# Kernel optimization log

Hardware: AMD Instinct MI355X
Metric: run time of the kernel (lower is better)

The kernel has to match this reference:

```python
import jax, jax.numpy as jnp
import numpy as np

EPS = 1e-5


def setup_inputs() -> dict:
    key = jax.random.key(0)
    x = jax.random.normal(key, (16, 128, 513), dtype=jnp.float32)
    return {"x": x}


def reference(x):
    N, C, T = x.shape
    # split into even / odd time indices
    x1 = x[:, :, 0::2]                      # (N, C, t) with t = ceil(T/2)
    x2 = x[:, :, 1::2]                      # (N, C, p) with p = floor(T/2)
    # outer-product score: exp(x1)[...,t] * exp(-x2)[...,p]  -> (N, C, t, p)
    g = jnp.exp(x1)[:, :, :, None] * jnp.exp(-x2)[:, :, None, :]
    g = jnp.log(g + EPS) ** 2
    # mean over channels, then exp -> (N, t, p)
    RAM = jnp.exp(jnp.sum(g, axis=1) / C)
    # normalizeRAM: threshold + sum-based symmetric normalization
    RAM = jnp.where(RAM < 0.5, jnp.zeros_like(RAM), RAM)
    da = jnp.sum(RAM, axis=1)               # (N, p)  sum over t
    db = jnp.sum(RAM, axis=2)               # (N, t)  sum over p
    norm = (db[:, :, None] * da[:, None, :] + EPS) ** -0.5
    RAM = RAM * norm                         # (N, t, p)
    # upsample by 2 along both dims, drop last row -> (N, T, T-1)
    RAM = jnp.repeat(RAM, 2, axis=1)[:, :-1, :]
    RAM = jnp.repeat(RAM, 2, axis=2)
    # einsum 'nct,ntp->nct' == x * sum_p RAM
    return x * jnp.sum(RAM, axis=2)[:, None, :]
```

## Files before the change

### kernel.cpp

```cpp
#include <hip/hip_runtime.h>
#include <math.h>

#define N_B 16
#define C_CH 128
#define T_LEN 513
#define NI 257
#define NJ 256
#define NPD 9
#define SCALE (1.4426950408889634f/128.0f)

typedef unsigned u32;
typedef unsigned short u16;
typedef short bf16x8 __attribute__((ext_vector_type(8)));
typedef float f32x4 __attribute__((ext_vector_type(4)));

#define RAM_F 0
#define PDA_F (N_B*NI*NJ)

__device__ inline u32 cvtpk(float a, float b) {
    u32 r;
    asm("v_cvt_pk_bf16_f32 %0, %1, %2" : "=v"(r) : "v"(a), "v"(b));
    return r;
}

__device__ inline void cvt8(const float* fa, bf16x8& hv, bf16x8& lv) {
    union { u32 w[4]; bf16x8 v; } H, L;
    #pragma unroll
    for (int p = 0; p < 4; ++p) {
        const float a = fa[2*p], b = fa[2*p+1];
        const u32 h = cvtpk(a, b);
        const float la = a - __builtin_bit_cast(float, h << 16);
        const float lb = b - __builtin_bit_cast(float, h & 0xffff0000u);
        H.w[p] = h;
        L.w[p] = cvtpk(la, lb);
    }
    hv = H.v; lv = L.v;
}

__global__ __launch_bounds__(512, 2) void k1(const float* __restrict__ x,
                                             float* __restrict__ ram,
                                             float* __restrict__ pda) {
    __shared__ float As[64][132];
    __shared__ float Bs[64][132];
    const int jb = blockIdx.x, ib = blockIdx.y, n = blockIdx.z;
    const int i0 = ib * 64, j0 = jb * 64;
    const int tid = threadIdx.x;
    const int l = tid & 63, wv = tid >> 6;
    const float* xn = x + (size_t)n * (C_CH * T_LEN);
    float* rn = ram + (size_t)n * NI * NJ;

    {
        #pragma unroll
        for (int m = 0; m < 16; ++m) {
            const int c = wv * 16 + m;
            {
                const int idx = c * T_LEN + 2 * i0 + 2 * l;
                const float2 f2 = *(const float2*)(xn + (idx & ~1));
                As[l][c] = (idx & 1) ? f2.y : f2.x;
            }
            {
                const int idx = c * T_LEN + 2 * j0 + 2 * l + 1;
                const float2 f2 = *(const float2*)(xn + (idx & ~1));
                Bs[l][c] = (idx & 1) ? f2.y : f2.x;
            }
        }
    }
    __syncthreads();

    const int il = l & 15, g = l >> 4;
    const int ia = wv >> 2, jt = wv & 3;
    {
        bf16x8 ah[2][4], al[2][4], bh[4], bl[4];
        float psum[2] = {0.f, 0.f}, qsq = 0.f;
        #pragma unroll
        for (int kc = 0; kc < 4; ++kc) {
            float fb[8];
            const float* bp = &Bs[jt * 16 + il][kc * 32 + 8 * g];
            #pragma unroll
            for (int e = 0; e < 8; ++e) fb[e] = bp[e];
            #pragma unroll
            for (int e = 0; e < 8; ++e) qsq = fmaf(fb[e], fb[e], qsq);
            cvt8(fb, bh[kc], bl[kc]);
            #pragma unroll
            for (int s = 0; s < 2; ++s) {
                float fa[8];
                const float* ap = &As[ia * 32 + s * 16 + il][kc * 32 + 8 * g];
                #pragma unroll
                for (int e = 0; e < 8; ++e) fa[e] = ap[e];
                #pragma unroll
                for (int e = 0; e < 8; ++e) psum[s] = fmaf(fa[e], fa[e], psum[s]);
                cvt8(fa, ah[s][kc], al[s][kc]);
            }
        }
        #pragma unroll
        for (int s = 0; s < 2; ++s) {
            psum[s] += __shfl_xor(psum[s], 16, 64);
            psum[s] += __shfl_xor(psum[s], 32, 64);
        }
        qsq += __shfl_xor(qsq, 16, 64);
        qsq += __shfl_xor(qsq, 32, 64);
        float pv[2][4];
        #pragma unroll
        for (int s = 0; s < 2; ++s)
            #pragma unroll
            for (int r = 0; r < 4; ++r) pv[s][r] = __shfl(psum[s], 4 * g + r, 64);

        f32x4 acc[2];
        acc[0] = (f32x4){0.f, 0.f, 0.f, 0.f};
        acc[1] = (f32x4){0.f, 0.f, 0.f, 0.f};
        #pragma unroll
        for (int kc = 0; kc < 4; ++kc) {
            #pragma unroll
            for (int s = 0; s < 2; ++s) {
                acc[s] = __builtin_amdgcn_mfma_f32_16x16x32_bf16(ah[s][kc], bh[kc], acc[s], 0, 0, 0);
                acc[s] = __builtin_amdgcn_mfma_f32_16x16x32_bf16(ah[s][kc], bl[kc], acc[s], 0, 0, 0);
                acc[s] = __builtin_amdgcn_mfma_f32_16x16x32_bf16(al[s][kc], bh[kc], acc[s], 0, 0, 0);
            }
        }
        const int j = j0 + jt * 16 + il;
        float cs = 0.f;
        #pragma unroll
        for (int s = 0; s < 2; ++s) {
            #pragma unroll
            for (int r = 0; r < 4; ++r) {
                const int i = i0 + ia * 32 + s * 16 + 4 * g + r;
                const float rv = exp2f((pv[s][r] + qsq - 2.f * acc[s][r]) * SCALE);
                rn[(size_t)i * NJ + j] = rv;
                cs += rv;
            }
        }
        cs += __shfl_xor(cs, 16, 64);
        cs += __shfl_xor(cs, 32, 64);
        if (l < 16) pda[((size_t)n * NPD + ib * 2 + ia) * NJ + j0 + jt * 16 + l] = cs;
    }

    if (ib == 0) {
        const int jl = tid >> 3, sub = tid & 7;
        float sab = 0.f, saa = 0.f, sbb = 0.f;
        #pragma unroll
        for (int e = 0; e < 16; ++e) {
            const int c = sub * 16 + e;
            const float a = xn[c * T_LEN + 512];
            const float b = Bs[jl][c];
            sab = fmaf(a, b, sab);
            saa = fmaf(a, a, saa);
            sbb = fmaf(b, b, sbb);
        }
        #pragma unroll
        for (int o = 4; o; o >>= 1) {
            sab += __shfl_xor(sab, o, 64);
            saa += __shfl_xor(saa, o, 64);
            sbb += __shfl_xor(sbb, o, 64);
        }
        if (sub == 0) {
            const float rv = exp2f((saa + sbb - 2.f * sab) * SCALE);
            rn[(size_t)256 * NJ + j0 + jl] = rv;
            pda[((size_t)n * NPD + 8) * NJ + j0 + jl] = rv;
        }
    }
}

__global__ __launch_bounds__(256) void k2(const float* __restrict__ ram,
                                          const float* __restrict__ pda,
                                          const float* __restrict__ x,
                                          float* __restrict__ out) {
    const int ic = blockIdx.x, n = blockIdx.y;
    __shared__ float w_s[NJ];
    __shared__ float f_s[16];
    const int tid = threadIdx.x;
    {
        float da = 0.f;
        #pragma unroll
        for (int k = 0; k < NPD; ++k) da += pda[((size_t)n * NPD + k) * NJ + tid];
        w_s[tid] = rsqrtf(da);
    }
    __syncthreads();
    const int wv = tid >> 6, lane = tid & 63;
    #pragma unroll
    for (int rr = 0; rr < 4; ++rr) {
        const int lr = wv * 4 + rr;
        const int i = ic * 16 + lr;
        if (i < NI) {
            const float* rrow = ram + ((size_t)n * NI + i) * NJ;
            float db = 0.f, t0 = 0.f;
            #pragma unroll
            for (int k = 0; k < 4; ++k) {
                const float v = rrow[lane + 64 * k];
                db += v;
                t0 = fmaf(v, w_s[lane + 64 * k], t0);
            }
            #pragma unroll
            for (int off = 32; off; off >>= 1) {
                db += __shfl_xor(db, off, 64);
                t0 += __shfl_xor(t0, off, 64);
            }
            if (lane == 0) f_s[lr] = 2.f * t0 * rsqrtf(db);
        }
    }
    __syncthreads();
    const int tt = tid & 31, cgp = tid >> 5;
    const int t = ic * 32 + tt;
    if (t < T_LEN) {
        const float f = f_s[tt >> 1];
        const float* xn = x + (size_t)n * C_CH * T_LEN;
        float* on = out + (size_t)n * C_CH * T_LEN;
        #pragma unroll
        for (int p = 0; p < 16; ++p) {
            const int c = cgp * 16 + p;
            on[c * T_LEN + t] = xn[c * T_LEN + t] * f;
        }
    }
}

extern "C" void kernel_launch(void* const* d_in, const int* in_sizes, int n_in,
                              void* d_out, int out_size, void* d_ws, size_t ws_size,
                              hipStream_t stream) {
    const float* x = (const float*)d_in[0];
    float* out = (float*)d_out;
    float* ws = (float*)d_ws;
    float* ram = ws + RAM_F;
    float* pda = ws + PDA_F;

    k1<<<dim3(4, 4, N_B), 512, 0, stream>>>(x, ram, pda);
    k2<<<dim3(17, N_B), 256, 0, stream>>>(ram, pda, x, out);
}
```

Measured before the change: 19.35 us.

## Convert operands to split bf16 once at load and store bf16 tiles in LDS

Each element is now split into high and low bf16 parts once, while loading from global memory, and stored as bf16 tiles in shared memory. Previously each wave re-read fp32 tiles and converted them redundantly. Row squared norms are now reduced through shared memory instead of wave shuffles, and MFMA fragments are read with vector LDS loads. This cuts redundant conversion and halves LDS traffic. It adds an extra barrier and reconstructs the last-column B values from the hi+lo parts, which is slightly less precise than the original fp32.

```diff
diff --git a/kernel.cpp b/kernel.cpp
--- a/kernel.cpp
+++ b/kernel.cpp
@@ -13,6 +13,7 @@
 typedef unsigned short u16;
 typedef short bf16x8 __attribute__((ext_vector_type(8)));
 typedef float f32x4 __attribute__((ext_vector_type(4)));
+typedef u32 u32x4 __attribute__((ext_vector_type(4)));
 
 #define RAM_F 0
 #define PDA_F (N_B*NI*NJ)
@@ -23,25 +24,12 @@
     return r;
 }
 
-__device__ inline void cvt8(const float* fa, bf16x8& hv, bf16x8& lv) {
-    union { u32 w[4]; bf16x8 v; } H, L;
-    #pragma unroll
-    for (int p = 0; p < 4; ++p) {
-        const float a = fa[2*p], b = fa[2*p+1];
-        const u32 h = cvtpk(a, b);
-        const float la = a - __builtin_bit_cast(float, h << 16);
-        const float lb = b - __builtin_bit_cast(float, h & 0xffff0000u);
-        H.w[p] = h;
-        L.w[p] = cvtpk(la, lb);
-    }
-    hv = H.v; lv = L.v;
-}
-
 __global__ __launch_bounds__(512, 2) void k1(const float* __restrict__ x,
                                              float* __restrict__ ram,
                                              float* __restrict__ pda) {
-    __shared__ float As[64][132];
-    __shared__ float Bs[64][132];
+    __shared__ u16 Ah[64][136], Al[64][136], Bh[64][136], Bl[64][136];
+    __shared__ float PpT[8][64], QpT[8][64];
+    __shared__ float Ps[64], Qs[64];
     const int jb = blockIdx.x, ib = blockIdx.y, n = blockIdx.z;
     const int i0 = ib * 64, j0 = jb * 64;
     const int tid = threadIdx.x;
@@ -50,89 +38,102 @@
     float* rn = ram + (size_t)n * NI * NJ;
 
     {
+        float av[16], bv[16];
         #pragma unroll
         for (int m = 0; m < 16; ++m) {
             const int c = wv * 16 + m;
             {
                 const int idx = c * T_LEN + 2 * i0 + 2 * l;
                 const float2 f2 = *(const float2*)(xn + (idx & ~1));
-                As[l][c] = (idx & 1) ? f2.y : f2.x;
+                av[m] = (idx & 1) ? f2.y : f2.x;
             }
             {
                 const int idx = c * T_LEN + 2 * j0 + 2 * l + 1;
                 const float2 f2 = *(const float2*)(xn + (idx & ~1));
-                Bs[l][c] = (idx & 1) ? f2.y : f2.x;
-            }
-        }
-    }
-    __syncthreads();
+                bv[m] = (idx & 1) ? f2.y : f2.x;
+            }
+        }
+        float pp = 0.f, qq = 0.f;
+        u32 ahw[8], alw[8], bhw[8], blw[8];
+        #pragma unroll
+        for (int p = 0; p < 8; ++p) {
+            const float a0 = av[2*p], a1 = av[2*p+1];
+            const float b0 = bv[2*p], b1 = bv[2*p+1];
+            pp = fmaf(a0, a0, fmaf(a1, a1, pp));
+            qq = fmaf(b0, b0, fmaf(b1, b1, qq));
+            const u32 ha = cvtpk(a0, a1);
+            ahw[p] = ha;
+            alw[p] = cvtpk(a0 - __builtin_bit_cast(float, ha << 16),
+                           a1 - __builtin_bit_cast(float, ha & 0xffff0000u));
+            const u32 hb = cvtpk(b0, b1);
+            bhw[p] = hb;
+            blw[p] = cvtpk(b0 - __builtin_bit_cast(float, hb << 16),
+                           b1 - __builtin_bit_cast(float, hb & 0xffff0000u));
+        }
+        u32* d;
+        d = (u32*)&Ah[l][16 * wv]; *(u32x4*)d = *(u32x4*)&ahw[0]; *(u32x4*)(d + 4) = *(u32x4*)&ahw[4];
+        d = (u32*)&Al[l][16 * wv]; *(u32x4*)d = *(u32x4*)&alw[0]; *(u32x4*)(d + 4) = *(u32x4*)&alw[4];
+        d = (u32*)&Bh[l][16 * wv]; *(u32x4*)d = *(u32x4*)&bhw[0]; *(u32x4*)(d + 4) = *(u32x4*)&bhw[4];
+        d = (u32*)&Bl[l][16 * wv]; *(u32x4*)d = *(u32x4*)&blw[0]; *(u32x4*)(d + 4) = *(u32x4*)&blw[4];
+        PpT[wv][l] = pp;
+        QpT[wv][l] = qq;
+    }
+    __syncthreads();
+
+    if (tid < 64) {
+        float s = 0.f;
+        #pragma unroll
+        for (int w = 0; w < 8; ++w) s += PpT[w][tid];
+        Ps[tid] = s;
+    } else if (tid < 128) {
+        float s = 0.f;
+        #pragma unroll
+        for (int w = 0; w < 8; ++w) s += QpT[w][tid - 64];
+        Qs[tid - 64] = s;
+    }
 
     const int il = l & 15, g = l >> 4;
     const int ia = wv >> 2, jt = wv & 3;
-    {
-        bf16x8 ah[2][4], al[2][4], bh[4], bl[4];
-        float psum[2] = {0.f, 0.f}, qsq = 0.f;
-        #pragma unroll
-        for (int kc = 0; kc < 4; ++kc) {
-            float fb[8];
-            const float* bp = &Bs[jt * 16 + il][kc * 32 + 8 * g];
-            #pragma unroll
-            for (int e = 0; e < 8; ++e) fb[e] = bp[e];
-            #pragma unroll
-            for (int e = 0; e < 8; ++e) qsq = fmaf(fb[e], fb[e], qsq);
-            cvt8(fb, bh[kc], bl[kc]);
-            #pragma unroll
-            for (int s = 0; s < 2; ++s) {
-                float fa[8];
-                const float* ap = &As[ia * 32 + s * 16 + il][kc * 32 + 8 * g];
-                #pragma unroll
-                for (int e = 0; e < 8; ++e) fa[e] = ap[e];
-                #pragma unroll
-                for (int e = 0; e < 8; ++e) psum[s] = fmaf(fa[e], fa[e], psum[s]);
-                cvt8(fa, ah[s][kc], al[s][kc]);
-            }
-        }
+    bf16x8 fah[2][4], fal[2][4], fbh[4], fbl[4];
+    #pragma unroll
+    for (int kc = 0; kc < 4; ++kc) {
+        fbh[kc]    = *(const bf16x8*)&Bh[jt * 16 + il][kc * 32 + 8 * g];
+        fbl[kc]    = *(const bf16x8*)&Bl[jt * 16 + il][kc * 32 + 8 * g];
+        fah[0][kc] = *(const bf16x8*)&Ah[ia * 32 + il][kc * 32 + 8 * g];
+        fah[1][kc] = *(const bf16x8*)&Ah[ia * 32 + 16 + il][kc * 32 + 8 * g];
+        fal[0][kc] = *(const bf16x8*)&Al[ia * 32 + il][kc * 32 + 8 * g];
+        fal[1][kc] = *(const bf16x8*)&Al[ia * 32 + 16 + il][kc * 32 + 8 * g];
+    }
+    f32x4 acc[2];
+    acc[0] = (f32x4){0.f, 0.f, 0.f, 0.f};
+    acc[1] = (f32x4){0.f, 0.f, 0.f, 0.f};
+    #pragma unroll
+    for (int kc = 0; kc < 4; ++kc) {
         #pragma unroll
         for (int s = 0; s < 2; ++s) {
-            psum[s] += __shfl_xor(psum[s], 16, 64);
-            psum[s] += __shfl_xor(psum[s], 32, 64);
-        }
-        qsq += __shfl_xor(qsq, 16, 64);
-        qsq += __shfl_xor(qsq, 32, 64);
-        float pv[2][4];
-        #pragma unroll
-        for (int s = 0; s < 2; ++s)
-            #pragma unroll
-            for (int r = 0; r < 4; ++r) pv[s][r] = __shfl(psum[s], 4 * g + r, 64);
-
-        f32x4 acc[2];
-        acc[0] = (f32x4){0.f, 0.f, 0.f, 0.f};
-        acc[1] = (f32x4){0.f, 0.f, 0.f, 0.f};
-        #pragma unroll
-        for (int kc = 0; kc < 4; ++kc) {
-            #pragma unroll
-            for (int s = 0; s < 2; ++s) {
-                acc[s] = __builtin_amdgcn_mfma_f32_16x16x32_bf16(ah[s][kc], bh[kc], acc[s], 0, 0, 0);
-                acc[s] = __builtin_amdgcn_mfma_f32_16x16x32_bf16(ah[s][kc], bl[kc], acc[s], 0, 0, 0);
-                acc[s] = __builtin_amdgcn_mfma_f32_16x16x32_bf16(al[s][kc], bh[kc], acc[s], 0, 0, 0);
-            }
-        }
-        const int j = j0 + jt * 16 + il;
-        float cs = 0.f;
-        #pragma unroll
-        for (int s = 0; s < 2; ++s) {
-            #pragma unroll
-            for (int r = 0; r < 4; ++r) {
-                const int i = i0 + ia * 32 + s * 16 + 4 * g + r;
-                const float rv = exp2f((pv[s][r] + qsq - 2.f * acc[s][r]) * SCALE);
-                rn[(size_t)i * NJ + j] = rv;
-                cs += rv;
-            }
-        }
-        cs += __shfl_xor(cs, 16, 64);
-        cs += __shfl_xor(cs, 32, 64);
-        if (l < 16) pda[((size_t)n * NPD + ib * 2 + ia) * NJ + j0 + jt * 16 + l] = cs;
-    }
+            acc[s] = __builtin_amdgcn_mfma_f32_16x16x32_bf16(fah[s][kc], fbh[kc], acc[s], 0, 0, 0);
+            acc[s] = __builtin_amdgcn_mfma_f32_16x16x32_bf16(fah[s][kc], fbl[kc], acc[s], 0, 0, 0);
+            acc[s] = __builtin_amdgcn_mfma_f32_16x16x32_bf16(fal[s][kc], fbh[kc], acc[s], 0, 0, 0);
+        }
+    }
+    __syncthreads();
+
+    const float qv = Qs[jt * 16 + il];
+    const int j = j0 + jt * 16 + il;
+    float cs = 0.f;
+    #pragma unroll
+    for (int s = 0; s < 2; ++s) {
+        #pragma unroll
+        for (int r = 0; r < 4; ++r) {
+            const int iloc = ia * 32 + s * 16 + 4 * g + r;
+            const float rv = exp2f((Ps[iloc] + qv - 2.f * acc[s][r]) * SCALE);
+            rn[(size_t)(i0 + iloc) * NJ + j] = rv;
+            cs += rv;
+        }
+    }
+    cs += __shfl_xor(cs, 16, 64);
+    cs += __shfl_xor(cs, 32, 64);
+    if (l < 16) pda[((size_t)n * NPD + ib * 2 + ia) * NJ + j0 + jt * 16 + l] = cs;
 
     if (ib == 0) {
         const int jl = tid >> 3, sub = tid & 7;
@@ -141,7 +142,8 @@
         for (int e = 0; e < 16; ++e) {
             const int c = sub * 16 + e;
             const float a = xn[c * T_LEN + 512];
-            const float b = Bs[jl][c];
+            const float b = __builtin_bit_cast(float, (u32)Bh[jl][c] << 16)
+                          + __builtin_bit_cast(float, (u32)Bl[jl][c] << 16);
             sab = fmaf(a, b, sab);
             saa = fmaf(a, a, saa);
             sbb = fmaf(b, b, sbb);
```

Result: no change. 19.26 us (-0.5%).
